# Kernel optimization log

Measured on AMD Instinct MI355X. Metric: run time of the kernel, lower is better.

Reference implementation:

```python
import jax, jax.numpy as jnp
import numpy as np
from jax import lax

T, B, H, W, C = 32, 32, 84, 84, 3
HID = 1024
A = 7
CONV_OUT = 32 * 11 * 11  # 84->42->21->11 with k3 s2 p1


def _elu(x):
    return jnp.where(x > 0, x, jnp.expm1(x))


def _conv(x, w, b):
    # x: [N, Cin, W, H], w: [Cout, Cin, 3, 3], stride 2, pad 1
    y = lax.conv_general_dilated(x, w, (2, 2), ((1, 1), (1, 1)),
                                 dimension_numbers=('NCHW', 'OIHW', 'NCHW'))
    return y + b[None, :, None, None]


def _lstm_cell(x, h, c, wih, whh, bih, bhh):
    # PyTorch gate order: i, f, g, o
    g = x @ wih.T + h @ whh.T + (bih + bhh)
    i, f, gg, o = jnp.split(g, 4, axis=-1)
    c_new = jax.nn.sigmoid(f) * c + jax.nn.sigmoid(i) * jnp.tanh(gg)
    h_new = jax.nn.sigmoid(o) * jnp.tanh(c_new)
    return h_new, c_new


def setup_inputs():
    key = jax.random.key(0)
    ks = jax.random.split(key, 24)
    rn = lambda k, s, sc=0.05: jax.random.normal(k, s, jnp.float32) * sc
    inp = {}
    inp['frame'] = jax.random.uniform(ks[0], (T, B, H, W, C), jnp.float32)
    inp['done'] = jnp.zeros((T, B), jnp.bool_)
    inp['h0'] = jnp.zeros((2, B, HID), jnp.float32)
    inp['c0'] = jnp.zeros((2, B, HID), jnp.float32)
    inp['conv_w1'] = rn(ks[1], (32, C, 3, 3), 0.1)
    inp['conv_b1'] = jnp.zeros((32,), jnp.float32)
    inp['conv_w2'] = rn(ks[2], (32, 32, 3, 3), 0.1)
    inp['conv_b2'] = jnp.zeros((32,), jnp.float32)
    inp['conv_w3'] = rn(ks[3], (32, 32, 3, 3), 0.1)
    inp['conv_b3'] = jnp.zeros((32,), jnp.float32)
    inp['fc_w1'] = rn(ks[4], (HID, CONV_OUT), 0.02)
    inp['fc_b1'] = jnp.zeros((HID,), jnp.float32)
    inp['fc_w2'] = rn(ks[5], (HID, HID), 0.02)
    inp['fc_b2'] = jnp.zeros((HID,), jnp.float32)
    inp['wih0'] = rn(ks[6], (4 * HID, HID), 0.02)
    inp['whh0'] = rn(ks[7], (4 * HID, HID), 0.02)
    inp['bih0'] = jnp.zeros((4 * HID,), jnp.float32)
    inp['bhh0'] = jnp.zeros((4 * HID,), jnp.float32)
    inp['wih1'] = rn(ks[8], (4 * HID, HID), 0.02)
    inp['whh1'] = rn(ks[9], (4 * HID, HID), 0.02)
    inp['bih1'] = jnp.zeros((4 * HID,), jnp.float32)
    inp['bhh1'] = jnp.zeros((4 * HID,), jnp.float32)
    inp['pol_w'] = rn(ks[10], (A, HID), 0.05)
    inp['pol_b'] = jnp.zeros((A,), jnp.float32)
    inp['base_w'] = rn(ks[11], (1, HID), 0.05)
    inp['base_b'] = jnp.zeros((1,), jnp.float32)
    return inp


def reference(frame, done, h0, c0,
              conv_w1, conv_b1, conv_w2, conv_b2, conv_w3, conv_b3,
              fc_w1, fc_b1, fc_w2, fc_b2,
              wih0, whh0, bih0, bhh0, wih1, whh1, bih1, bhh1,
              pol_w, pol_b, base_w, base_b):
    t, b = frame.shape[0], frame.shape[1]
    x = frame.reshape(t * b, H, W, C).astype(jnp.float32)
    x = jnp.transpose(x, (0, 3, 2, 1))  # torch transpose(1,3): [TB, C, W, H]
    x = _elu(_conv(x, conv_w1, conv_b1))
    x = _elu(_conv(x, conv_w2, conv_b2))
    x = _elu(_conv(x, conv_w3, conv_b3))
    x = x.reshape(t * b, -1)
    x = jax.nn.relu(x @ fc_w1.T + fc_b1)
    x = jax.nn.relu(x @ fc_w2.T + fc_b2)
    core_input = x.reshape(t, b, HID)
    notdone = (1.0 - done.astype(jnp.float32))[:, :, None]  # [T, B, 1]

    def step(carry, xs):
        h, c = carry  # [2, B, HID]
        xt, nd = xs
        h = h * nd[None]
        c = c * nd[None]
        h0n, c0n = _lstm_cell(xt, h[0], c[0], wih0, whh0, bih0, bhh0)
        h1n, c1n = _lstm_cell(h0n, h[1], c[1], wih1, whh1, bih1, bhh1)
        return (jnp.stack([h0n, h1n]), jnp.stack([c0n, c1n])), h1n

    (h_fin, c_fin), core_out = lax.scan(step, (h0, c0), (core_input, notdone))
    core_out = core_out.reshape(t * b, HID)
    logits = core_out @ pol_w.T + pol_b
    baseline = core_out @ base_w.T + base_b
    action = jnp.argmax(logits, axis=1)  # eval-mode action selection
    policy_logits = logits.reshape(t, b, A)
    baseline = baseline.reshape(t, b)
    action = action.reshape(t, b)
    return policy_logits, baseline, action, h_fin, c_fin
```

## Files before the change

### kernel.cpp

```cpp
#include <hip/hip_runtime.h>
#include <cmath>



__device__ __forceinline__ float eluf(float v) {
    return v > 0.f ? v : expm1f(v);
}

__global__ __launch_bounds__(256) void repack_w(const float* __restrict__ w1,
    const float* __restrict__ w2, const float* __restrict__ w3, float* __restrict__ wt)
{
    int i = blockIdx.x * 256 + threadIdx.x;
    if (i < 864) {
        int co = i & 31, r = i >> 5;
        int tap = r / 3, ci = r - tap * 3;
        int k1 = tap / 3, k2 = tap - k1 * 3;
        wt[i] = w1[co * 27 + ci * 9 + k1 * 3 + k2];
    } else if (i < 10080) {
        int o = i - 864;
        int co = o & 31, r = o >> 5;
        int tap = r >> 5, ci = r & 31;
        int k1 = tap / 3, k2 = tap - k1 * 3;
        wt[i] = w2[co * 288 + ci * 9 + k1 * 3 + k2];
    } else if (i < 19296) {
        int o = i - 10080;
        int co = o & 31, r = o >> 5;
        int tap = r >> 5, ci = r & 31;
        int k1 = tap / 3, k2 = tap - k1 * 3;
        wt[i] = w3[co * 288 + ci * 9 + k1 * 3 + k2];
    }
}

__global__ __launch_bounds__(256) void bsum_k(const float* __restrict__ bih0,
    const float* __restrict__ bhh0, const float* __restrict__ bih1,
    const float* __restrict__ bhh1, float* __restrict__ bsum)
{
    int i = blockIdx.x * 256 + threadIdx.x;
    if (i < 4096) bsum[i] = bih0[i] + bhh0[i];
    else if (i < 8192) bsum[i] = bih1[i - 4096] + bhh1[i - 4096];
}

__global__ __launch_bounds__(256) void conv1_k(const float* __restrict__ frame,
    const float* __restrict__ w1t, const float* __restrict__ b1,
    float* __restrict__ out, int n0)
{
    __shared__ float As[27][132];
    __shared__ float Bs[27][32];
    int tid = threadIdx.x;
    if (tid < 216) ((float4*)Bs)[tid] = ((const float4*)w1t)[tid];

    int p0 = blockIdx.x << 7;
    int pxl = tid & 127;
    int half = tid >> 7;
    {
        int p = p0 + pxl;
        int nl = p / 1764;
        int rem = p - nl * 1764;
        int ox = rem / 42;
        int oy = rem - ox * 42;
        const float* fr = frame + (size_t)(n0 + nl) * 21168;
        for (int tap = half; tap < 9; tap += 2) {
            int k1 = tap / 3, k2 = tap - k1 * 3;
            int u = 2 * ox - 1 + k1;
            int v = 2 * oy - 1 + k2;
            bool ok = (u >= 0) && (u < 84) && (v >= 0) && (v < 84);
            int uc = ok ? u : 0, vc = ok ? v : 0;
            const float* fp = fr + (vc * 84 + uc) * 3;
            float x0 = fp[0], x1 = fp[1], x2 = fp[2];
            if (!ok) { x0 = 0.f; x1 = 0.f; x2 = 0.f; }
            As[tap * 3 + 0][pxl] = x0;
            As[tap * 3 + 1][pxl] = x1;
            As[tap * 3 + 2][pxl] = x2;
        }
    }
    __syncthreads();

    int tx = tid & 7, ty = tid >> 3;
    float acc[4][4];
#pragma unroll
    for (int i = 0; i < 4; i++)
#pragma unroll
        for (int j = 0; j < 4; j++) acc[i][j] = 0.f;

#pragma unroll 9
    for (int k = 0; k < 27; k++) {
        float4 a = *(const float4*)&As[k][ty << 2];
        float4 b = *(const float4*)&Bs[k][tx << 2];
        acc[0][0] = fmaf(a.x, b.x, acc[0][0]); acc[0][1] = fmaf(a.x, b.y, acc[0][1]);
        acc[0][2] = fmaf(a.x, b.z, acc[0][2]); acc[0][3] = fmaf(a.x, b.w, acc[0][3]);
        acc[1][0] = fmaf(a.y, b.x, acc[1][0]); acc[1][1] = fmaf(a.y, b.y, acc[1][1]);
        acc[1][2] = fmaf(a.y, b.z, acc[1][2]); acc[1][3] = fmaf(a.y, b.w, acc[1][3]);
        acc[2][0] = fmaf(a.z, b.x, acc[2][0]); acc[2][1] = fmaf(a.z, b.y, acc[2][1]);
        acc[2][2] = fmaf(a.z, b.z, acc[2][2]); acc[2][3] = fmaf(a.z, b.w, acc[2][3]);
        acc[3][0] = fmaf(a.w, b.x, acc[3][0]); acc[3][1] = fmaf(a.w, b.y, acc[3][1]);
        acc[3][2] = fmaf(a.w, b.z, acc[3][2]); acc[3][3] = fmaf(a.w, b.w, acc[3][3]);
    }

    float4 bc = *(const float4*)(b1 + (tx << 2));
#pragma unroll
    for (int i = 0; i < 4; i++) {
        float4 o;
        o.x = eluf(acc[i][0] + bc.x);
        o.y = eluf(acc[i][1] + bc.y);
        o.z = eluf(acc[i][2] + bc.z);
        o.w = eluf(acc[i][3] + bc.w);
        *(float4*)(out + (size_t)(p0 + (ty << 2) + i) * 32 + (tx << 2)) = o;
    }
}

template<int IS, int OS>
__global__ __launch_bounds__(256) void convg_k(const float* __restrict__ in,
    const float* __restrict__ wtb, const float* __restrict__ bias,
    float* __restrict__ out, int pOff)
{
    __shared__ float Bs[288 * 32];
    __shared__ float As[32][132];
    int tid = threadIdx.x;
    {
        const float4* src = (const float4*)wtb;
        float4* dst = (float4*)Bs;
#pragma unroll
        for (int r = 0; r < 9; r++) dst[tid + r * 256] = src[tid + r * 256];
    }
    const int OS2 = OS * OS;
    int p0 = blockIdx.x << 7;
    int c4 = tid & 7;
    int pn[4], pox[4], poy[4];
#pragma unroll
    for (int i = 0; i < 4; i++) {
        int px = (tid >> 3) + (i << 5);
        int p = p0 + px;
        int n = p / OS2;
        int rem = p - n * OS2;
        int ox = rem / OS;
        pn[i] = n; pox[i] = ox; poy[i] = rem - ox * OS;
    }

    int tx = tid & 7, ty = tid >> 3;
    float acc[4][4];
#pragma unroll
    for (int i = 0; i < 4; i++)
#pragma unroll
        for (int j = 0; j < 4; j++) acc[i][j] = 0.f;

    for (int k1 = 0; k1 < 3; k1++) {
        for (int k2 = 0; k2 < 3; k2++) {
            __syncthreads();
#pragma unroll
            for (int i = 0; i < 4; i++) {
                int px = (tid >> 3) + (i << 5);
                int u = 2 * pox[i] - 1 + k1;
                int v = 2 * poy[i] - 1 + k2;
                bool ok = (u >= 0) && (u < IS) && (v >= 0) && (v < IS);
                int uc = ok ? u : 0, vc = ok ? v : 0;
                float4 val = *(const float4*)(in +
                    ((size_t)((pn[i] * IS + uc) * IS + vc)) * 32 + (c4 << 2));
                if (!ok) { val.x = 0.f; val.y = 0.f; val.z = 0.f; val.w = 0.f; }
                As[(c4 << 2) + 0][px] = val.x;
                As[(c4 << 2) + 1][px] = val.y;
                As[(c4 << 2) + 2][px] = val.z;
                As[(c4 << 2) + 3][px] = val.w;
            }
            __syncthreads();
            const float* bsrc = Bs + (size_t)((k1 * 3 + k2) << 5) * 32;
#pragma unroll 8
            for (int k = 0; k < 32; k++) {
                float4 a = *(const float4*)&As[k][ty << 2];
                float4 b = *(const float4*)&bsrc[(k << 5) + (tx << 2)];
                acc[0][0] = fmaf(a.x, b.x, acc[0][0]); acc[0][1] = fmaf(a.x, b.y, acc[0][1]);
                acc[0][2] = fmaf(a.x, b.z, acc[0][2]); acc[0][3] = fmaf(a.x, b.w, acc[0][3]);
                acc[1][0] = fmaf(a.y, b.x, acc[1][0]); acc[1][1] = fmaf(a.y, b.y, acc[1][1]);
                acc[1][2] = fmaf(a.y, b.z, acc[1][2]); acc[1][3] = fmaf(a.y, b.w, acc[1][3]);
                acc[2][0] = fmaf(a.z, b.x, acc[2][0]); acc[2][1] = fmaf(a.z, b.y, acc[2][1]);
                acc[2][2] = fmaf(a.z, b.z, acc[2][2]); acc[2][3] = fmaf(a.z, b.w, acc[2][3]);
                acc[3][0] = fmaf(a.w, b.x, acc[3][0]); acc[3][1] = fmaf(a.w, b.y, acc[3][1]);
                acc[3][2] = fmaf(a.w, b.z, acc[3][2]); acc[3][3] = fmaf(a.w, b.w, acc[3][3]);
            }
        }
    }

    float4 bc = *(const float4*)(bias + (tx << 2));
#pragma unroll
    for (int i = 0; i < 4; i++) {
        float4 o;
        o.x = eluf(acc[i][0] + bc.x);
        o.y = eluf(acc[i][1] + bc.y);
        o.z = eluf(acc[i][2] + bc.z);
        o.w = eluf(acc[i][3] + bc.w);
        *(float4*)(out + (size_t)(pOff + p0 + (ty << 2) + i) * 32 + (tx << 2)) = o;
    }
}

__global__ __launch_bounds__(256) void repack_fw1(const float* __restrict__ fw1,
    float* __restrict__ fw1t)
{
    __shared__ float row[3872];
    int h = blockIdx.x;
    const float* src = fw1 + (size_t)h * 3872;
    for (int j = threadIdx.x; j < 3872; j += 256) row[j] = src[j];
    __syncthreads();
    float* dst = fw1t + (size_t)h * 3872;
    for (int j = threadIdx.x; j < 3872; j += 256) {
        int p = j >> 5, co = j & 31;
        dst[j] = row[co * 121 + p];
    }
}

__global__ __launch_bounds__(256) void gemm128(const float* __restrict__ A,
    const float* __restrict__ Bm, float* __restrict__ Cbase, size_t Cstride,
    int N, int K, int Nt, int kchunk)
{
    __shared__ float As[2][16][132];
    __shared__ float Bs[2][16][132];
    int tid = threadIdx.x;
    int bid = blockIdx.x;
    int nt = bid % Nt, mt = bid / Nt;
    int n0 = nt << 7, m0 = mt << 7;
    int kbeg = blockIdx.z * kchunk;
    int kend = kbeg + kchunk;
    if (kend > K) kend = K;
    int T = (kend - kbeg) >> 4;
    float* C = Cbase + (size_t)blockIdx.z * Cstride;

    int tx = tid & 15, ty = tid >> 4;
    int r0 = tid >> 2, kc0 = (tid & 3) << 2;
    int r1 = (tid + 256) >> 2, kc1 = kc0;
    const float* a0p = A + (size_t)(m0 + r0) * K + kbeg + kc0;
    const float* a1p = A + (size_t)(m0 + r1) * K + kbeg + kc1;
    const float* b0p = Bm + (size_t)(n0 + r0) * K + kbeg + kc0;
    const float* b1p = Bm + (size_t)(n0 + r1) * K + kbeg + kc1;

    float acc[8][8];
#pragma unroll
    for (int i = 0; i < 8; i++)
#pragma unroll
        for (int j = 0; j < 8; j++) acc[i][j] = 0.f;

    float4 pa0 = *(const float4*)a0p;
    float4 pa1 = *(const float4*)a1p;
    float4 pb0 = *(const float4*)b0p;
    float4 pb1 = *(const float4*)b1p;
    As[0][kc0 + 0][r0] = pa0.x; As[0][kc0 + 1][r0] = pa0.y;
    As[0][kc0 + 2][r0] = pa0.z; As[0][kc0 + 3][r0] = pa0.w;
    As[0][kc1 + 0][r1] = pa1.x; As[0][kc1 + 1][r1] = pa1.y;
    As[0][kc1 + 2][r1] = pa1.z; As[0][kc1 + 3][r1] = pa1.w;
    Bs[0][kc0 + 0][r0] = pb0.x; Bs[0][kc0 + 1][r0] = pb0.y;
    Bs[0][kc0 + 2][r0] = pb0.z; Bs[0][kc0 + 3][r0] = pb0.w;
    Bs[0][kc1 + 0][r1] = pb1.x; Bs[0][kc1 + 1][r1] = pb1.y;
    Bs[0][kc1 + 2][r1] = pb1.z; Bs[0][kc1 + 3][r1] = pb1.w;

    int p = 0;
    for (int t = 0; t < T; t++) {
        __syncthreads();
        bool more = (t + 1 < T);
        if (more) {
            int ko = (t + 1) << 4;
            pa0 = *(const float4*)(a0p + ko);
            pa1 = *(const float4*)(a1p + ko);
            pb0 = *(const float4*)(b0p + ko);
            pb1 = *(const float4*)(b1p + ko);
        }
#pragma unroll
        for (int k = 0; k < 16; k++) {
            float a[8], b[8];
            *(float4*)&a[0] = *(const float4*)&As[p][k][ty << 2];
            *(float4*)&a[4] = *(const float4*)&As[p][k][64 + (ty << 2)];
            *(float4*)&b[0] = *(const float4*)&Bs[p][k][tx << 2];
            *(float4*)&b[4] = *(const float4*)&Bs[p][k][64 + (tx << 2)];
#pragma unroll
            for (int i = 0; i < 8; i++)
#pragma unroll
                for (int j = 0; j < 8; j++) acc[i][j] = fmaf(a[i], b[j], acc[i][j]);
        }
        if (more) {
            int q = p ^ 1;
            As[q][kc0 + 0][r0] = pa0.x; As[q][kc0 + 1][r0] = pa0.y;
            As[q][kc0 + 2][r0] = pa0.z; As[q][kc0 + 3][r0] = pa0.w;
            As[q][kc1 + 0][r1] = pa1.x; As[q][kc1 + 1][r1] = pa1.y;
            As[q][kc1 + 2][r1] = pa1.z; As[q][kc1 + 3][r1] = pa1.w;
            Bs[q][kc0 + 0][r0] = pb0.x; Bs[q][kc0 + 1][r0] = pb0.y;
            Bs[q][kc0 + 2][r0] = pb0.z; Bs[q][kc0 + 3][r0] = pb0.w;
            Bs[q][kc1 + 0][r1] = pb1.x; Bs[q][kc1 + 1][r1] = pb1.y;
            Bs[q][kc1 + 2][r1] = pb1.z; Bs[q][kc1 + 3][r1] = pb1.w;
            p = q;
        }
    }

#pragma unroll
    for (int i = 0; i < 8; i++) {
        int row = m0 + ((i < 4) ? ((ty << 2) + i) : (64 + (ty << 2) + i - 4));
        float* cp0 = C + (size_t)row * N + n0 + (tx << 2);
        float4 s0; s0.x = acc[i][0]; s0.y = acc[i][1]; s0.z = acc[i][2]; s0.w = acc[i][3];
        float4 s1; s1.x = acc[i][4]; s1.y = acc[i][5]; s1.z = acc[i][6]; s1.w = acc[i][7];
        *(float4*)cp0 = s0;
        *(float4*)(cp0 + 64) = s1;
    }
}

__global__ __launch_bounds__(256) void bias_relu_sum(const float* __restrict__ p,
    size_t stride, int nz, const float* __restrict__ b, float* __restrict__ out)
{
    int i = blockIdx.x * 256 + threadIdx.x;
    float v = b[i & 1023];
    for (int z = 0; z < nz; z++) v += p[i + (size_t)z * stride];
    out[i] = v > 0.f ? v : 0.f;
}

__global__ __launch_bounds__(256) void lstm_step(
    const float* __restrict__ gxa,
    const float* __restrict__ gxb,
    const float* __restrict__ whh,
    const float* __restrict__ bsum,
    const float* __restrict__ hprev,
    const float* __restrict__ cprev,
    float* __restrict__ cout,
    float* __restrict__ Hout,
    const unsigned char* __restrict__ dmask,
    int t)
{
    __shared__ float Hs[32][132];
    __shared__ float Ws[8][132];
    __shared__ float4 part[16][65];
    int tid = threadIdx.x;
    int bg = tid & 7;
    int u  = (tid >> 3) & 1;
    int s  = tid >> 4;
    int jb = (int)blockIdx.x << 1;
    int r0 = tid >> 5;
    int c40 = tid & 31;

    float nds[4];
#pragma unroll
    for (int rep = 0; rep < 4; rep++) nds[rep] = dmask[r0 + (rep << 3)] ? 0.f : 1.f;

    int wuu = tid >> 7, wg = (tid >> 5) & 3, wc = tid & 31;
    const float* wsrc = whh + ((size_t)(wg << 10) + jb + wuu) * 1024 + (wc << 2);

    float acc[4][4];
#pragma unroll
    for (int i = 0; i < 4; i++)
#pragma unroll
        for (int g = 0; g < 4; g++) acc[i][g] = 0.f;

    for (int kt = 0; kt < 8; kt++) {
        if (kt) __syncthreads();
#pragma unroll
        for (int rep = 0; rep < 4; rep++) {
            int r = r0 + (rep << 3);
            float4 h4 = *(const float4*)(hprev + (size_t)r * 1024 + (kt << 7) + (c40 << 2));
            float nd = nds[rep];
            h4.x *= nd; h4.y *= nd; h4.z *= nd; h4.w *= nd;
            *(float4*)&Hs[r][(c40 ^ ((r >> 2) & 7)) << 2] = h4;
        }
        *(float4*)&Ws[(wuu << 2) + wg][wc << 2] = *(const float4*)(wsrc + (kt << 7));
        __syncthreads();
#pragma unroll
        for (int kq = 0; kq < 2; kq++) {
            int col4 = (s << 1) + kq;
            float4 w0 = *(const float4*)&Ws[(u << 2) + 0][col4 << 2];
            float4 w1 = *(const float4*)&Ws[(u << 2) + 1][col4 << 2];
            float4 w2 = *(const float4*)&Ws[(u << 2) + 2][col4 << 2];
            float4 w3 = *(const float4*)&Ws[(u << 2) + 3][col4 << 2];
#pragma unroll
            for (int i = 0; i < 4; i++) {
                float4 h4 = *(const float4*)&Hs[(bg << 2) + i][(col4 ^ bg) << 2];
                acc[i][0] = fmaf(h4.x, w0.x, fmaf(h4.y, w0.y, fmaf(h4.z, w0.z, fmaf(h4.w, w0.w, acc[i][0]))));
                acc[i][1] = fmaf(h4.x, w1.x, fmaf(h4.y, w1.y, fmaf(h4.z, w1.z, fmaf(h4.w, w1.w, acc[i][1]))));
                acc[i][2] = fmaf(h4.x, w2.x, fmaf(h4.y, w2.y, fmaf(h4.z, w2.z, fmaf(h4.w, w2.w, acc[i][2]))));
                acc[i][3] = fmaf(h4.x, w3.x, fmaf(h4.y, w3.y, fmaf(h4.z, w3.z, fmaf(h4.w, w3.w, acc[i][3]))));
            }
        }
    }

#pragma unroll
    for (int i = 0; i < 4; i++) {
        float4 pv; pv.x = acc[i][0]; pv.y = acc[i][1]; pv.z = acc[i][2]; pv.w = acc[i][3];
        part[s][(((bg << 2) + i) << 1) + u] = pv;
    }
    __syncthreads();
    if (tid < 64) {
        int b = tid & 31, uu = tid >> 5;
        float4 sum; sum.x = 0.f; sum.y = 0.f; sum.z = 0.f; sum.w = 0.f;
#pragma unroll
        for (int sl = 0; sl < 16; sl++) {
            float4 pv = part[sl][(b << 1) + uu];
            sum.x += pv.x; sum.y += pv.y; sum.z += pv.z; sum.w += pv.w;
        }
        int j = jb + uu;
        int row = (t << 5) + b;
        const float* gpa = gxa + (size_t)row * 4096 + j;
        const float* gpb = gxb + (size_t)row * 4096 + j;
        float g0 = sum.x + gpa[0]    + gpb[0]    + bsum[j];
        float g1 = sum.y + gpa[1024] + gpb[1024] + bsum[j + 1024];
        float g2 = sum.z + gpa[2048] + gpb[2048] + bsum[j + 2048];
        float g3 = sum.w + gpa[3072] + gpb[3072] + bsum[j + 3072];
        float nd = dmask[b] ? 0.f : 1.f;
        float cp = cprev[(size_t)b * 1024 + j] * nd;
        float si = 1.f / (1.f + expf(-g0));
        float sf = 1.f / (1.f + expf(-g1));
        float so = 1.f / (1.f + expf(-g3));
        float cn = sf * cp + si * tanhf(g2);
        float hn = so * tanhf(cn);
        cout[(size_t)b * 1024 + j] = cn;
        Hout[(size_t)row * 1024 + j] = hn;
    }
}

__global__ __launch_bounds__(256) void heads_k(const float* __restrict__ Hc,
    const float* __restrict__ pw, const float* __restrict__ pb,
    const float* __restrict__ bw, const float* __restrict__ bbias,
    float* __restrict__ out)
{
    __shared__ float red[8][264];
    int n = blockIdx.x, tid = threadIdx.x;
    float4 x4 = *(const float4*)(Hc + (size_t)n * 1024 + (tid << 2));
#pragma unroll
    for (int a = 0; a < 7; a++) {
        float4 w4 = *(const float4*)(pw + (size_t)a * 1024 + (tid << 2));
        red[a][tid] = x4.x * w4.x + x4.y * w4.y + x4.z * w4.z + x4.w * w4.w;
    }
    {
        float4 w4 = *(const float4*)(bw + (tid << 2));
        red[7][tid] = x4.x * w4.x + x4.y * w4.y + x4.z * w4.z + x4.w * w4.w;
    }
    __syncthreads();
    for (int off = 128; off > 0; off >>= 1) {
        if (tid < off) {
#pragma unroll
            for (int a = 0; a < 8; a++) red[a][tid] += red[a][tid + off];
        }
        __syncthreads();
    }
    if (tid == 0) {
        float best = -1e30f; int bi = 0;
        for (int a = 0; a < 7; a++) {
            float L = red[a][0] + pb[a];
            out[n * 7 + a] = L;
            if (L > best) { best = L; bi = a; }
        }
        out[7168 + n] = red[7][0] + bbias[0];
        out[8192 + n] = (float)bi;
    }
}

__global__ __launch_bounds__(256) void final_copy(const float* __restrict__ H0,
    const float* __restrict__ H1, const float* __restrict__ cst, float* __restrict__ out)
{
    int i = blockIdx.x * 256 + threadIdx.x;
    if (i < 65536) {
        int l = i >> 15;
        int rem = i & 32767;
        const float* H = l ? H1 : H0;
        out[9216 + i] = H[(size_t)(31 * 32) * 1024 + rem];
    } else {
        out[74752 + (i - 65536)] = cst[i - 65536];
    }
}

extern "C" void kernel_launch(void* const* d_in, const int* in_sizes, int n_in,
                              void* d_out, int out_size, void* d_ws, size_t ws_size,
                              hipStream_t stream)
{
    (void)in_sizes; (void)n_in; (void)out_size; (void)ws_size;
    const float* frame = (const float*)d_in[0];
    const unsigned char* done8 = (const unsigned char*)d_in[1];
    const float* h0   = (const float*)d_in[2];
    const float* c0   = (const float*)d_in[3];
    const float* cw1  = (const float*)d_in[4];
    const float* cb1  = (const float*)d_in[5];
    const float* cw2  = (const float*)d_in[6];
    const float* cb2  = (const float*)d_in[7];
    const float* cw3  = (const float*)d_in[8];
    const float* cb3  = (const float*)d_in[9];
    const float* fw1  = (const float*)d_in[10];
    const float* fb1  = (const float*)d_in[11];
    const float* fw2  = (const float*)d_in[12];
    const float* fb2  = (const float*)d_in[13];
    const float* wih0 = (const float*)d_in[14];
    const float* whh0 = (const float*)d_in[15];
    const float* bih0 = (const float*)d_in[16];
    const float* bhh0 = (const float*)d_in[17];
    const float* wih1 = (const float*)d_in[18];
    const float* whh1 = (const float*)d_in[19];
    const float* bih1 = (const float*)d_in[20];
    const float* bhh1 = (const float*)d_in[21];
    const float* pw   = (const float*)d_in[22];
    const float* pb   = (const float*)d_in[23];
    const float* bw   = (const float*)d_in[24];
    const float* bbias= (const float*)d_in[25];

    float* ws   = (float*)d_ws;
    float* A    = ws;
    float* Bv   = A + 14450688;
    float* fc1  = Bv + 7225344;
    float* cin  = fc1 + 1048576;
    float* H0   = cin + 1048576;
    float* H1   = H0 + 1048576;
    float* cst  = H1 + 1048576;
    float* bsum = cst + 65536;
    float* wt   = bsum + 8192;
    float* fw1t = A + 8388608;
    float* fcp  = A;
    float* gxp  = A;
    float* conv2f = A;
    float* conv3o = Bv;
    float* out = (float*)d_out;

    repack_w<<<76, 256, 0, stream>>>(cw1, cw2, cw3, wt);
    bsum_k<<<32, 256, 0, stream>>>(bih0, bhh0, bih1, bhh1, bsum);

    for (int ch = 0; ch < 8; ch++) {
        conv1_k<<<1764, 256, 0, stream>>>(frame, wt, cb1, Bv, ch * 128);
        convg_k<42, 21><<<441, 256, 0, stream>>>(Bv, wt + 864, cb2, conv2f, ch * 128 * 441);
    }
    convg_k<21, 11><<<968, 256, 0, stream>>>(conv2f, wt + 10080, cb3, conv3o, 0);
    repack_fw1<<<1024, 256, 0, stream>>>(fw1, fw1t);

    { dim3 g(64, 1, 8); gemm128<<<g, 256, 0, stream>>>(conv3o, fw1t, fcp, 1048576, 1024, 3872, 8, 496); }
    bias_relu_sum<<<4096, 256, 0, stream>>>(fcp, 1048576, 8, fb1, fc1);
    { dim3 g(64, 1, 8); gemm128<<<g, 256, 0, stream>>>(fc1, fw2, fcp, 1048576, 1024, 1024, 8, 128); }
    bias_relu_sum<<<4096, 256, 0, stream>>>(fcp, 1048576, 8, fb2, cin);

    { dim3 g(256, 1, 2); gemm128<<<g, 256, 0, stream>>>(cin, wih0, gxp, 4194304, 4096, 1024, 32, 512); }
    for (int t = 0; t < 32; t++) {
        const float* hp = t ? (H0 + (size_t)(t - 1) * 32768) : h0;
        const float* cp = t ? cst : c0;
        lstm_step<<<512, 256, 0, stream>>>(gxp, gxp + 4194304, whh0, bsum, hp, cp, cst, H0, done8 + t * 32, t);
    }
    { dim3 g(256, 1, 2); gemm128<<<g, 256, 0, stream>>>(H0, wih1, gxp, 4194304, 4096, 1024, 32, 512); }
    for (int t = 0; t < 32; t++) {
        const float* hp = t ? (H1 + (size_t)(t - 1) * 32768) : (h0 + 32768);
        const float* cp = t ? (cst + 32768) : (c0 + 32768);
        lstm_step<<<512, 256, 0, stream>>>(gxp, gxp + 4194304, whh1, bsum + 4096, hp, cp, cst + 32768, H1, done8 + t * 32, t);
    }
    heads_k<<<1024, 256, 0, stream>>>(H1, pw, pb, bw, bbias, out);
    final_copy<<<512, 256, 0, stream>>>(H0, H1, cst, out);
}
```

Before: 1.886 ms.

## Replace FP32 SIMT GEMMs with split-bf16 MFMA GEMMs (3-pass hi/lo)

The FP32 register-tiled GEMM is replaced with an MFMA kernel. Each operand is split into bf16 hi and lo parts, and three bf16 MFMA products (lo*hi, hi*lo, hi*hi) approximate FP32 accuracy. New conversion kernels pre-split the activations and weights. The split-K counts change, and the input-projection GEMMs now run without split-K, so lstm_step reads a single gx buffer. The cost is extra conversion passes and memory traffic. The kernel also reads operands straight from global memory without LDS staging, which may limit reuse.

```diff
diff --git a/kernel.cpp b/kernel.cpp
--- a/kernel.cpp
+++ b/kernel.cpp
@@ -3,8 +3,24 @@
 
 
 
+typedef short bf16x8 __attribute__((ext_vector_type(8)));
+typedef float f32x4 __attribute__((ext_vector_type(4)));
+
 __device__ __forceinline__ float eluf(float v) {
     return v > 0.f ? v : expm1f(v);
+}
+
+__device__ __forceinline__ unsigned short f2bf(float x) {
+    unsigned int u = __float_as_uint(x);
+    u += 0x7FFFu + ((u >> 16) & 1u);
+    return (unsigned short)(u >> 16);
+}
+
+__device__ __forceinline__ void bfsplit(float x, unsigned short& h, unsigned short& l) {
+    unsigned short hb = f2bf(x);
+    float hf = __uint_as_float((unsigned int)hb << 16);
+    h = hb;
+    l = f2bf(x - hf);
 }
 
 __global__ __launch_bounds__(256) void repack_w(const float* __restrict__ w1,
@@ -38,6 +54,26 @@
     int i = blockIdx.x * 256 + threadIdx.x;
     if (i < 4096) bsum[i] = bih0[i] + bhh0[i];
     else if (i < 8192) bsum[i] = bih1[i - 4096] + bhh1[i - 4096];
+}
+
+__global__ __launch_bounds__(256) void cvt_split(const float* __restrict__ src,
+    unsigned short* __restrict__ hi, unsigned short* __restrict__ lo, int n)
+{
+    int i = (blockIdx.x * 256 + threadIdx.x) << 3;
+    if (i >= n) return;
+    float4 v0 = *(const float4*)(src + i);
+    float4 v1 = *(const float4*)(src + i + 4);
+    float vs[8] = {v0.x, v0.y, v0.z, v0.w, v1.x, v1.y, v1.z, v1.w};
+    bf16x8 hv, lv;
+#pragma unroll
+    for (int j = 0; j < 8; j++) {
+        unsigned short hb, lb;
+        bfsplit(vs[j], hb, lb);
+        hv[j] = (short)hb;
+        lv[j] = (short)lb;
+    }
+    *(bf16x8*)(hi + i) = hv;
+    *(bf16x8*)(lo + i) = lv;
 }
 
 __global__ __launch_bounds__(256) void conv1_k(const float* __restrict__ frame,
@@ -192,108 +228,99 @@
 }
 
 __global__ __launch_bounds__(256) void repack_fw1(const float* __restrict__ fw1,
-    float* __restrict__ fw1t)
+    unsigned short* __restrict__ hi, unsigned short* __restrict__ lo)
 {
     __shared__ float row[3872];
     int h = blockIdx.x;
     const float* src = fw1 + (size_t)h * 3872;
     for (int j = threadIdx.x; j < 3872; j += 256) row[j] = src[j];
     __syncthreads();
-    float* dst = fw1t + (size_t)h * 3872;
+    unsigned short* dh = hi + (size_t)h * 3872;
+    unsigned short* dl = lo + (size_t)h * 3872;
     for (int j = threadIdx.x; j < 3872; j += 256) {
         int p = j >> 5, co = j & 31;
-        dst[j] = row[co * 121 + p];
-    }
-}
-
-__global__ __launch_bounds__(256) void gemm128(const float* __restrict__ A,
-    const float* __restrict__ Bm, float* __restrict__ Cbase, size_t Cstride,
-    int N, int K, int Nt, int kchunk)
-{
-    __shared__ float As[2][16][132];
-    __shared__ float Bs[2][16][132];
+        unsigned short hb, lb;
+        bfsplit(row[co * 121 + p], hb, lb);
+        dh[j] = hb;
+        dl[j] = lb;
+    }
+}
+
+__global__ __launch_bounds__(256) void gemm_mfma(
+    const unsigned short* __restrict__ Ahi, const unsigned short* __restrict__ Alo,
+    const unsigned short* __restrict__ Bhi, const unsigned short* __restrict__ Blo,
+    float* __restrict__ Cbase, size_t Cstride, int N, int K, int Nt, int kchunk)
+{
     int tid = threadIdx.x;
+    int w = tid >> 6, l = tid & 63;
     int bid = blockIdx.x;
     int nt = bid % Nt, mt = bid / Nt;
-    int n0 = nt << 7, m0 = mt << 7;
+    int m0 = mt << 6, n0 = nt << 7;
     int kbeg = blockIdx.z * kchunk;
     int kend = kbeg + kchunk;
     if (kend > K) kend = K;
-    int T = (kend - kbeg) >> 4;
+    int steps = (kend - kbeg) >> 5;
     float* C = Cbase + (size_t)blockIdx.z * Cstride;
 
-    int tx = tid & 15, ty = tid >> 4;
-    int r0 = tid >> 2, kc0 = (tid & 3) << 2;
-    int r1 = (tid + 256) >> 2, kc1 = kc0;
-    const float* a0p = A + (size_t)(m0 + r0) * K + kbeg + kc0;
-    const float* a1p = A + (size_t)(m0 + r1) * K + kbeg + kc1;
-    const float* b0p = Bm + (size_t)(n0 + r0) * K + kbeg + kc0;
-    const float* b1p = Bm + (size_t)(n0 + r1) * K + kbeg + kc1;
-
-    float acc[8][8];
-#pragma unroll
-    for (int i = 0; i < 8; i++)
-#pragma unroll
-        for (int j = 0; j < 8; j++) acc[i][j] = 0.f;
-
-    float4 pa0 = *(const float4*)a0p;
-    float4 pa1 = *(const float4*)a1p;
-    float4 pb0 = *(const float4*)b0p;
-    float4 pb1 = *(const float4*)b1p;
-    As[0][kc0 + 0][r0] = pa0.x; As[0][kc0 + 1][r0] = pa0.y;
-    As[0][kc0 + 2][r0] = pa0.z; As[0][kc0 + 3][r0] = pa0.w;
-    As[0][kc1 + 0][r1] = pa1.x; As[0][kc1 + 1][r1] = pa1.y;
-    As[0][kc1 + 2][r1] = pa1.z; As[0][kc1 + 3][r1] = pa1.w;
-    Bs[0][kc0 + 0][r0] = pb0.x; Bs[0][kc0 + 1][r0] = pb0.y;
-    Bs[0][kc0 + 2][r0] = pb0.z; Bs[0][kc0 + 3][r0] = pb0.w;
-    Bs[0][kc1 + 0][r1] = pb1.x; Bs[0][kc1 + 1][r1] = pb1.y;
-    Bs[0][kc1 + 2][r1] = pb1.z; Bs[0][kc1 + 3][r1] = pb1.w;
-
-    int p = 0;
-    for (int t = 0; t < T; t++) {
-        __syncthreads();
-        bool more = (t + 1 < T);
-        if (more) {
-            int ko = (t + 1) << 4;
-            pa0 = *(const float4*)(a0p + ko);
-            pa1 = *(const float4*)(a1p + ko);
-            pb0 = *(const float4*)(b0p + ko);
-            pb1 = *(const float4*)(b1p + ko);
-        }
-#pragma unroll
-        for (int k = 0; k < 16; k++) {
-            float a[8], b[8];
-            *(float4*)&a[0] = *(const float4*)&As[p][k][ty << 2];
-            *(float4*)&a[4] = *(const float4*)&As[p][k][64 + (ty << 2)];
-            *(float4*)&b[0] = *(const float4*)&Bs[p][k][tx << 2];
-            *(float4*)&b[4] = *(const float4*)&Bs[p][k][64 + (tx << 2)];
-#pragma unroll
-            for (int i = 0; i < 8; i++)
-#pragma unroll
-                for (int j = 0; j < 8; j++) acc[i][j] = fmaf(a[i], b[j], acc[i][j]);
-        }
-        if (more) {
-            int q = p ^ 1;
-            As[q][kc0 + 0][r0] = pa0.x; As[q][kc0 + 1][r0] = pa0.y;
-            As[q][kc0 + 2][r0] = pa0.z; As[q][kc0 + 3][r0] = pa0.w;
-            As[q][kc1 + 0][r1] = pa1.x; As[q][kc1 + 1][r1] = pa1.y;
-            As[q][kc1 + 2][r1] = pa1.z; As[q][kc1 + 3][r1] = pa1.w;
-            Bs[q][kc0 + 0][r0] = pb0.x; Bs[q][kc0 + 1][r0] = pb0.y;
-            Bs[q][kc0 + 2][r0] = pb0.z; Bs[q][kc0 + 3][r0] = pb0.w;
-            Bs[q][kc1 + 0][r1] = pb1.x; Bs[q][kc1 + 1][r1] = pb1.y;
-            Bs[q][kc1 + 2][r1] = pb1.z; Bs[q][kc1 + 3][r1] = pb1.w;
-            p = q;
-        }
-    }
-
-#pragma unroll
-    for (int i = 0; i < 8; i++) {
-        int row = m0 + ((i < 4) ? ((ty << 2) + i) : (64 + (ty << 2) + i - 4));
-        float* cp0 = C + (size_t)row * N + n0 + (tx << 2);
-        float4 s0; s0.x = acc[i][0]; s0.y = acc[i][1]; s0.z = acc[i][2]; s0.w = acc[i][3];
-        float4 s1; s1.x = acc[i][4]; s1.y = acc[i][5]; s1.z = acc[i][6]; s1.w = acc[i][7];
-        *(float4*)cp0 = s0;
-        *(float4*)(cp0 + 64) = s1;
+    int wm = (w & 1) << 5;
+    int wn = (w >> 1) << 6;
+    int lr = l & 15;
+    int lk = (l >> 4) << 3;
+
+    size_t aoff = (size_t)(m0 + wm + lr) * K + kbeg + lk;
+    size_t boff = (size_t)(n0 + wn + lr) * K + kbeg + lk;
+    const unsigned short* pah = Ahi + aoff;
+    const unsigned short* pal = Alo + aoff;
+    const unsigned short* pbh = Bhi + boff;
+    const unsigned short* pbl = Blo + boff;
+    const size_t rstr = (size_t)16 * K;
+
+    f32x4 acc[2][4];
+#pragma unroll
+    for (int i = 0; i < 2; i++)
+#pragma unroll
+        for (int j = 0; j < 4; j++) acc[i][j] = (f32x4){0.f, 0.f, 0.f, 0.f};
+
+    for (int s = 0; s < steps; s++) {
+        int ko = s << 5;
+        bf16x8 ah0 = *(const bf16x8*)(pah + ko);
+        bf16x8 ah1 = *(const bf16x8*)(pah + rstr + ko);
+        bf16x8 al0 = *(const bf16x8*)(pal + ko);
+        bf16x8 al1 = *(const bf16x8*)(pal + rstr + ko);
+        bf16x8 bh[4], bl[4];
+#pragma unroll
+        for (int c = 0; c < 4; c++) {
+            bh[c] = *(const bf16x8*)(pbh + (size_t)c * rstr + ko);
+            bl[c] = *(const bf16x8*)(pbl + (size_t)c * rstr + ko);
+        }
+#pragma unroll
+        for (int c = 0; c < 4; c++) {
+            acc[0][c] = __builtin_amdgcn_mfma_f32_16x16x32_bf16(al0, bh[c], acc[0][c], 0, 0, 0);
+            acc[1][c] = __builtin_amdgcn_mfma_f32_16x16x32_bf16(al1, bh[c], acc[1][c], 0, 0, 0);
+        }
+#pragma unroll
+        for (int c = 0; c < 4; c++) {
+            acc[0][c] = __builtin_amdgcn_mfma_f32_16x16x32_bf16(ah0, bl[c], acc[0][c], 0, 0, 0);
+            acc[1][c] = __builtin_amdgcn_mfma_f32_16x16x32_bf16(ah1, bl[c], acc[1][c], 0, 0, 0);
+        }
+#pragma unroll
+        for (int c = 0; c < 4; c++) {
+            acc[0][c] = __builtin_amdgcn_mfma_f32_16x16x32_bf16(ah0, bh[c], acc[0][c], 0, 0, 0);
+            acc[1][c] = __builtin_amdgcn_mfma_f32_16x16x32_bf16(ah1, bh[c], acc[1][c], 0, 0, 0);
+        }
+    }
+
+    int rrow = (l >> 4) << 2;
+#pragma unroll
+    for (int ri = 0; ri < 2; ri++) {
+#pragma unroll
+        for (int ci = 0; ci < 4; ci++) {
+            int row = m0 + wm + (ri << 4) + rrow;
+            int col = n0 + wn + (ci << 4) + lr;
+            float* cp = C + (size_t)row * N + col;
+#pragma unroll
+            for (int r = 0; r < 4; r++) cp[(size_t)r * N] = acc[ri][ci][r];
+        }
     }
 }
 
@@ -307,8 +334,7 @@
 }
 
 __global__ __launch_bounds__(256) void lstm_step(
-    const float* __restrict__ gxa,
-    const float* __restrict__ gxb,
+    const float* __restrict__ gx,
     const float* __restrict__ whh,
     const float* __restrict__ bsum,
     const float* __restrict__ hprev,
@@ -388,12 +414,11 @@
         }
         int j = jb + uu;
         int row = (t << 5) + b;
-        const float* gpa = gxa + (size_t)row * 4096 + j;
-        const float* gpb = gxb + (size_t)row * 4096 + j;
-        float g0 = sum.x + gpa[0]    + gpb[0]    + bsum[j];
-        float g1 = sum.y + gpa[1024] + gpb[1024] + bsum[j + 1024];
-        float g2 = sum.z + gpa[2048] + gpb[2048] + bsum[j + 2048];
-        float g3 = sum.w + gpa[3072] + gpb[3072] + bsum[j + 3072];
+        const float* gp = gx + (size_t)row * 4096 + j;
+        float g0 = sum.x + gp[0]    + bsum[j];
+        float g1 = sum.y + gp[1024] + bsum[j + 1024];
+        float g2 = sum.z + gp[2048] + bsum[j + 2048];
+        float g3 = sum.w + gp[3072] + bsum[j + 3072];
         float nd = dmask[b] ? 0.f : 1.f;
         float cp = cprev[(size_t)b * 1024 + j] * nd;
         float si = 1.f / (1.f + expf(-g0));
@@ -499,11 +524,27 @@
     float* cst  = H1 + 1048576;
     float* bsum = cst + 65536;
     float* wt   = bsum + 8192;
-    float* fw1t = A + 8388608;
-    float* fcp  = A;
-    float* gxp  = A;
     float* conv2f = A;
     float* conv3o = Bv;
+    unsigned short* c3hi = (unsigned short*)(A);
+    unsigned short* c3lo = (unsigned short*)(A + 1982464);
+    unsigned short* f1hi = (unsigned short*)(A + 3964928);
+    unsigned short* f1lo = (unsigned short*)(A + 5947392);
+    float* fc1p = Bv;
+    unsigned short* fc1hi = (unsigned short*)(Bv);
+    unsigned short* fc1lo = (unsigned short*)(Bv + 524288);
+    unsigned short* fw2hi = (unsigned short*)(Bv + 1048576);
+    unsigned short* fw2lo = (unsigned short*)(Bv + 1572864);
+    float* fc2p = A;
+    unsigned short* cinhi = (unsigned short*)(Bv + 2097152);
+    unsigned short* cinlo = (unsigned short*)(Bv + 2621440);
+    unsigned short* h0hi  = (unsigned short*)(Bv + 3145728);
+    unsigned short* h0lo  = (unsigned short*)(Bv + 3670016);
+    unsigned short* w0hi = (unsigned short*)(A);
+    unsigned short* w0lo = (unsigned short*)(A + 2097152);
+    unsigned short* w1hi = (unsigned short*)(A + 4194304);
+    unsigned short* w1lo = (unsigned short*)(A + 6291456);
+    float* gx = A + 8388608;
     float* out = (float*)d_out;
 
     repack_w<<<76, 256, 0, stream>>>(cw1, cw2, cw3, wt);
@@ -514,24 +555,37 @@
         convg_k<42, 21><<<441, 256, 0, stream>>>(Bv, wt + 864, cb2, conv2f, ch * 128 * 441);
     }
     convg_k<21, 11><<<968, 256, 0, stream>>>(conv2f, wt + 10080, cb3, conv3o, 0);
-    repack_fw1<<<1024, 256, 0, stream>>>(fw1, fw1t);
-
-    { dim3 g(64, 1, 8); gemm128<<<g, 256, 0, stream>>>(conv3o, fw1t, fcp, 1048576, 1024, 3872, 8, 496); }
-    bias_relu_sum<<<4096, 256, 0, stream>>>(fcp, 1048576, 8, fb1, fc1);
-    { dim3 g(64, 1, 8); gemm128<<<g, 256, 0, stream>>>(fc1, fw2, fcp, 1048576, 1024, 1024, 8, 128); }
-    bias_relu_sum<<<4096, 256, 0, stream>>>(fcp, 1048576, 8, fb2, cin);
-
-    { dim3 g(256, 1, 2); gemm128<<<g, 256, 0, stream>>>(cin, wih0, gxp, 4194304, 4096, 1024, 32, 512); }
+
+    cvt_split<<<1936, 256, 0, stream>>>(conv3o, c3hi, c3lo, 3964928);
+    repack_fw1<<<1024, 256, 0, stream>>>(fw1, f1hi, f1lo);
+
+    { dim3 g(128, 1, 6); gemm_mfma<<<g, 256, 0, stream>>>(c3hi, c3lo, f1hi, f1lo,
+        fc1p, 1048576, 1024, 3872, 8, 672); }
+    bias_relu_sum<<<4096, 256, 0, stream>>>(fc1p, 1048576, 6, fb1, fc1);
+
+    cvt_split<<<512, 256, 0, stream>>>(fc1, fc1hi, fc1lo, 1048576);
+    cvt_split<<<512, 256, 0, stream>>>(fw2, fw2hi, fw2lo, 1048576);
+    { dim3 g(128, 1, 4); gemm_mfma<<<g, 256, 0, stream>>>(fc1hi, fc1lo, fw2hi, fw2lo,
+        fc2p, 1048576, 1024, 1024, 8, 256); }
+    bias_relu_sum<<<4096, 256, 0, stream>>>(fc2p, 1048576, 4, fb2, cin);
+
+    cvt_split<<<512, 256, 0, stream>>>(cin, cinhi, cinlo, 1048576);
+    cvt_split<<<2048, 256, 0, stream>>>(wih0, w0hi, w0lo, 4194304);
+    cvt_split<<<2048, 256, 0, stream>>>(wih1, w1hi, w1lo, 4194304);
+    { dim3 g(512, 1, 1); gemm_mfma<<<g, 256, 0, stream>>>(cinhi, cinlo, w0hi, w0lo,
+        gx, 0, 4096, 1024, 32, 1024); }
     for (int t = 0; t < 32; t++) {
         const float* hp = t ? (H0 + (size_t)(t - 1) * 32768) : h0;
         const float* cp = t ? cst : c0;
-        lstm_step<<<512, 256, 0, stream>>>(gxp, gxp + 4194304, whh0, bsum, hp, cp, cst, H0, done8 + t * 32, t);
-    }
-    { dim3 g(256, 1, 2); gemm128<<<g, 256, 0, stream>>>(H0, wih1, gxp, 4194304, 4096, 1024, 32, 512); }
+        lstm_step<<<512, 256, 0, stream>>>(gx, whh0, bsum, hp, cp, cst, H0, done8 + t * 32, t);
+    }
+    cvt_split<<<512, 256, 0, stream>>>(H0, h0hi, h0lo, 1048576);
+    { dim3 g(512, 1, 1); gemm_mfma<<<g, 256, 0, stream>>>(h0hi, h0lo, w1hi, w1lo,
+        gx, 0, 4096, 1024, 32, 1024); }
     for (int t = 0; t < 32; t++) {
         const float* hp = t ? (H1 + (size_t)(t - 1) * 32768) : (h0 + 32768);
         const float* cp = t ? (cst + 32768) : (c0 + 32768);
-        lstm_step<<<512, 256, 0, stream>>>(gxp, gxp + 4194304, whh1, bsum + 4096, hp, cp, cst + 32768, H1, done8 + t * 32, t);
+        lstm_step<<<512, 256, 0, stream>>>(gx, whh1, bsum + 4096, hp, cp, cst + 32768, H1, done8 + t * 32, t);
     }
     heads_k<<<1024, 256, 0, stream>>>(H1, pw, pb, bw, bbias, out);
     final_copy<<<512, 256, 0, stream>>>(H0, H1, cst, out);
```

Result: faster. 1.704 ms (-9.7%).
